# Performance work log

Measured on AMD Instinct MI355X. Metric: run time of the kernel, lower is better.

## Reference

```python
import jax, jax.numpy as jnp
import numpy as np

N_NODES = 100000
N_EDGES = 1600000
INPUT_DIM = 512
HIDDEN = 64
N_LAYERS = 3


def setup_inputs() -> dict:
    key = jax.random.key(0)
    ks = jax.random.split(key, 8)
    s = 0.05
    return {
        "x": jax.random.normal(ks[0], (N_NODES, INPUT_DIM), jnp.float32),
        "edge_index": jax.random.randint(ks[1], (2, N_EDGES), 0, N_NODES, jnp.int64),
        "W_enc": jax.random.normal(ks[2], (INPUT_DIM, HIDDEN), jnp.float32) * s,
        "b_enc": jnp.zeros((HIDDEN,), jnp.float32),
        "Wl": jax.random.normal(ks[3], (N_LAYERS, HIDDEN, HIDDEN), jnp.float32) * s,
        "bl": jnp.zeros((N_LAYERS, HIDDEN), jnp.float32),
        "Wr": jax.random.normal(ks[4], (N_LAYERS, HIDDEN, HIDDEN), jnp.float32) * s,
        "W_cls": jax.random.normal(ks[5], (HIDDEN, 1), jnp.float32) * s,
        "b_cls": jnp.zeros((1,), jnp.float32),
    }


def reference(x, edge_index, W_enc, b_enc, Wl, bl, Wr, W_cls, b_cls):
    # node encoder
    h = x @ W_enc + b_enc  # [N, H]
    N = h.shape[0]
    src, dst = edge_index[0], edge_index[1]  # messages flow src -> dst (PyG convention)
    ones = jnp.ones((src.shape[0],), h.dtype)
    deg = jax.ops.segment_sum(ones, dst, num_segments=N)  # in-degree per node
    inv_deg = jnp.where(deg > 0, 1.0 / jnp.maximum(deg, 1.0), 0.0)[:, None]
    n_layers = Wl.shape[0]
    for l in range(n_layers):
        # SAGEConv: mean-aggregate neighbor features, transform, add root transform
        msgs = h[src]  # [E, H] gather
        agg = jax.ops.segment_sum(msgs, dst, num_segments=N) * inv_deg  # mean aggr
        h_new = agg @ Wl[l] + bl[l] + h @ Wr[l]
        h = jax.nn.relu(h + h_new)  # residual + relu
    out = jax.nn.sigmoid(h @ W_cls + b_cls)  # [N, 1]
    return out.squeeze(-1)
```

## Files before the change

### kernel.cpp

```cpp
#include <hip/hip_runtime.h>
#include <math.h>

#define HID 64
#define KIN 512
#define NBK_MAX 256

typedef __attribute__((ext_vector_type(8))) short short8;
typedef __attribute__((ext_vector_type(4))) float floatx4;
typedef __attribute__((ext_vector_type(2))) float floatx2;

__device__ inline unsigned bf16pair(float a, float b) {
  unsigned ua = __float_as_uint(a);
  unsigned ub = __float_as_uint(b);
  ua = (ua + 0x7FFFu + ((ua >> 16) & 1u)) >> 16;
  ub = (ub + 0x7FFFu + ((ub >> 16) & 1u)) >> 16;
  return ua | (ub << 16);
}
__device__ inline unsigned short bf16one(float a) {
  unsigned ua = __float_as_uint(a);
  return (unsigned short)((ua + 0x7FFFu + ((ua >> 16) & 1u)) >> 16);
}
__device__ inline unsigned char fp8q(float a) {
  const int pk = __builtin_amdgcn_cvt_pk_fp8_f32(a, a, 0, false);
  return (unsigned char)(pk & 0xff);
}

__global__ __launch_bounds__(1024) void prep_bucket_kernel(
    const float* __restrict__ We, const float* __restrict__ Wl,
    const float* __restrict__ Wr, unsigned short* __restrict__ wte,
    unsigned short* __restrict__ wlrt, const int* __restrict__ src,
    const int* __restrict__ dst, int* __restrict__ gcur,
    unsigned* __restrict__ ebuf, int E, int N, int NBK, int CAP) {
  const int blk = blockIdx.x;
  const int tid = threadIdx.x;
  if (blk < 32) {
    const int t = blk * 1024 + tid;
    const int c = t >> 9, k = t & 511;
    wte[c * KIN + k] = bf16one(We[k * HID + c]);
    return;
  }
  if (blk < 56) {
    const int t = (blk - 32) * 1024 + tid;
    if (t < 24576) {
      const int mat = t >> 12;
      const int e = t & 4095;
      const int c = e >> 6, k = e & 63;
      const float* sp = (mat < 3) ? (Wl + (size_t)mat * 4096)
                                  : (Wr + (size_t)(mat - 3) * 4096);
      wlrt[(size_t)mat * 4096 + c * 64 + k] = bf16one(sp[k * 64 + c]);
    }
    return;
  }
  __shared__ int hist[NBK_MAX];
  __shared__ int bbase[NBK_MAX];
  __shared__ int curloc[NBK_MAX];
  const int e0 = (blk - 56) * 4096;
  for (int i = tid; i < NBK; i += 1024) {
    hist[i] = 0;
    curloc[i] = 0;
  }
  __syncthreads();
  int bk[4];
  unsigned pk[4];
#pragma unroll
  for (int u = 0; u < 4; u++) {
    const int e = e0 + u * 1024 + tid;
    bk[u] = -1;
    pk[u] = 0;
    if (e < E) {
      const int d = dst[e];
      if ((unsigned)d < (unsigned)N) {
        int s = src[e];
        if ((unsigned)s >= (unsigned)N) s = 0;
        bk[u] = d >> 9;
        pk[u] = ((unsigned)s << 9) | (unsigned)(d & 511);
        atomicAdd(&hist[bk[u]], 1);
      }
    }
  }
  __syncthreads();
  for (int i = tid; i < NBK; i += 1024)
    if (hist[i]) bbase[i] = atomicAdd(&gcur[i], hist[i]);
  __syncthreads();
#pragma unroll
  for (int u = 0; u < 4; u++) {
    if (bk[u] >= 0) {
      const int gp = bbase[bk[u]] + atomicAdd(&curloc[bk[u]], 1);
      if (gp < CAP) ebuf[(size_t)bk[u] * CAP + gp] = pk[u];
    }
  }
}

__global__ __launch_bounds__(256) void scatter_enc_kernel(
    const unsigned* __restrict__ ebuf, const int* __restrict__ gcur,
    int* __restrict__ row_start, float* __restrict__ inv_deg,
    int* __restrict__ csr_src, const float* __restrict__ x,
    const unsigned short* __restrict__ wt, const float* __restrict__ b,
    unsigned short* __restrict__ hb, unsigned char* __restrict__ h8, int N,
    int NBK, int CAP) {
  __shared__ __align__(16) unsigned char smem[16384];
  if (blockIdx.x < (unsigned)NBK) {
    int* cur = (int*)smem;
    int* rsl = (int*)(smem + 2048);
    int* psc = (int*)(smem + 4096);
    int* soffp = (int*)(smem + 5120);
    const int bkt = blockIdx.x;
    const int nodeBase = bkt << 9;
    const int tid = threadIdx.x;
    cur[tid] = 0;
    cur[tid + 256] = 0;
    __syncthreads();
    int cnt_b = gcur[bkt];
    if (cnt_b > CAP) cnt_b = CAP;
    const unsigned* eb = ebuf + (size_t)bkt * CAP;
    for (int i = tid; i < cnt_b; i += 256) atomicAdd(&cur[eb[i] & 511], 1);
    if (tid < 64) {
      int s = 0;
      for (int b2 = tid; b2 < bkt; b2 += 64) s += gcur[b2];
#pragma unroll
      for (int off = 32; off > 0; off >>= 1) s += __shfl_down(s, off, 64);
      if (tid == 0) *soffp = s;
    }
    __syncthreads();
    const int d0 = cur[2 * tid];
    const int d1 = cur[2 * tid + 1];
    psc[tid] = d0 + d1;
    __syncthreads();
    for (int off = 1; off < 256; off <<= 1) {
      int t = (tid >= off) ? psc[tid - off] : 0;
      __syncthreads();
      psc[tid] += t;
      __syncthreads();
    }
    const int soff = *soffp;
    const int base0 = soff + psc[tid] - (d0 + d1);
    rsl[2 * tid] = base0;
    rsl[2 * tid + 1] = base0 + d0;
    const int g0 = nodeBase + 2 * tid;
    const int g1 = g0 + 1;
    if (g0 < N) {
      row_start[g0] = base0;
      inv_deg[g0] = d0 ? 1.0f / (float)d0 : 0.f;
    }
    if (g1 < N) {
      row_start[g1] = base0 + d0;
      inv_deg[g1] = d1 ? 1.0f / (float)d1 : 0.f;
    }
    if (bkt == NBK - 1 && tid == 255) row_start[N] = soff + psc[255];
    cur[tid] = 0;
    cur[tid + 256] = 0;
    __syncthreads();
    for (int i = tid; i < cnt_b; i += 256) {
      const unsigned p = eb[i];
      const int dl = p & 511;
      const int pos = rsl[dl] + atomicAdd(&cur[dl], 1);
      csr_src[pos] = (int)(p >> 9);
    }
    return;
  }
  uint4(*sx)[256] = (uint4(*)[256])smem;
  uint4(*sw)[256] = (uint4(*)[256])(smem + 8192);
  const int t = threadIdx.x;
  const int lane = t & 63;
  const int wid = t >> 6;
  const int m15 = lane & 15;
  const int quad = lane >> 4;
  const int blockBase = (blockIdx.x - NBK) * 64;

  const int rs = t >> 2;
  const int qs = t & 3;
  const int us = rs * 4 + (qs ^ ((rs >> 1) & 3));
  const int gn = blockBase + rs;
  const bool valid = gn < N;
  const float* xp = x + (size_t)(valid ? gn : 0) * KIN + qs * 8;
  const unsigned short* wp = wt + (size_t)rs * KIN + qs * 8;

  const int arow = wid * 16 + m15;
  const int ua = arow * 4 + (quad ^ ((arow >> 1) & 3));
  int ub[4];
#pragma unroll
  for (int c4 = 0; c4 < 4; c4++) {
    const int col = c4 * 16 + m15;
    ub[c4] = col * 4 + (quad ^ ((col >> 1) & 3));
  }

  floatx4 acc[4];
#pragma unroll
  for (int c4 = 0; c4 < 4; c4++)
#pragma unroll
    for (int j = 0; j < 4; j++) acc[c4][j] = 0.f;

  float4 fx0, fx1;
  uint4 wv;
  if (valid) {
    fx0 = *(const float4*)(xp);
    fx1 = *(const float4*)(xp + 4);
  } else {
    fx0 = fx1 = make_float4(0.f, 0.f, 0.f, 0.f);
  }
  wv = *(const uint4*)(wp);

  for (int kc = 0; kc < 16; kc++) {
    const int curb = kc & 1;
    uint4 xu;
    xu.x = bf16pair(fx0.x, fx0.y);
    xu.y = bf16pair(fx0.z, fx0.w);
    xu.z = bf16pair(fx1.x, fx1.y);
    xu.w = bf16pair(fx1.z, fx1.w);
    sx[curb][us] = xu;
    sw[curb][us] = wv;
    __syncthreads();
    if (kc < 15) {
      const int ko = (kc + 1) * 32;
      if (valid) {
        fx0 = *(const float4*)(xp + ko);
        fx1 = *(const float4*)(xp + ko + 4);
      }
      wv = *(const uint4*)(wp + ko);
    }
    const short8 a = __builtin_bit_cast(short8, sx[curb][ua]);
#pragma unroll
    for (int c4 = 0; c4 < 4; c4++) {
      const short8 bf = __builtin_bit_cast(short8, sw[curb][ub[c4]]);
      acc[c4] =
          __builtin_amdgcn_mfma_f32_16x16x32_bf16(a, bf, acc[c4], 0, 0, 0);
    }
  }

#pragma unroll
  for (int c4 = 0; c4 < 4; c4++) {
    const float bias = b[c4 * 16 + m15];
#pragma unroll
    for (int r = 0; r < 4; r++) {
      const int row = blockBase + wid * 16 + quad * 4 + r;
      if (row < N) {
        const float v = acc[c4][r] + bias;
        hb[(size_t)row * HID + c4 * 16 + m15] = bf16one(v);
        h8[(size_t)row * HID + c4 * 16 + m15] = fp8q(v);
      }
    }
  }
}

__global__ __launch_bounds__(256) void layer_kernel(
    const unsigned short* __restrict__ hin,
    const unsigned char* __restrict__ h8in, unsigned short* __restrict__ hout,
    unsigned char* __restrict__ h8out, const int* __restrict__ row_start,
    const int* __restrict__ csr_src, const float* __restrict__ inv_deg,
    const unsigned short* __restrict__ Wlt,
    const unsigned short* __restrict__ Wrt, const float* __restrict__ bl,
    const float* __restrict__ Wc, const float* __restrict__ bc,
    float* __restrict__ out, int N) {
  __shared__ uint4 sAgg[512];
  __shared__ uint4 sH[512];
  __shared__ uint4 sWl[512];
  __shared__ uint4 sWr[512];
  const int tid = threadIdx.x;
  const int lane = tid & 63;
  const int wid = tid >> 6;
  const int m15 = lane & 15;
  const int quad = lane >> 4;
  const int blockBase = blockIdx.x * 64;

  {
    const int r = tid >> 2;
    const int gp = tid & 3;
    const int g0 = gp * 2, g1 = gp * 2 + 1;
    const int u0 = r * 8 + (g0 ^ (r & 7));
    const int u1 = r * 8 + (g1 ^ (r & 7));
    const int gn = blockBase + r;
    if (gn < N) {
      const uint4* hp = (const uint4*)(hin + (size_t)gn * HID);
      sH[u0] = hp[g0];
      sH[u1] = hp[g1];
    } else {
      const uint4 z = make_uint4(0, 0, 0, 0);
      sH[u0] = z;
      sH[u1] = z;
    }
    const uint4* wl = (const uint4*)(Wlt + (size_t)r * HID);
    const uint4* wr = (const uint4*)(Wrt + (size_t)r * HID);
    sWl[u0] = wl[g0];
    sWl[u1] = wl[g1];
    sWr[u0] = wr[g0];
    sWr[u1] = wr[g1];
  }

  {
    const int slot = lane >> 2;
    const int qc = lane & 3;
    const int nl = wid * 16 + slot;
    const int gn = blockBase + nl;
    float a[16];
#pragma unroll
    for (int c = 0; c < 16; c++) a[c] = 0.f;
    float id = 0.f;
    if (gn < N) {
      id = inv_deg[gn];
      const int s = row_start[gn];
      const int e = row_start[gn + 1];
      for (int j = s; j < e; j += 8) {
        int n[8];
        bool ok[8];
#pragma unroll
        for (int u = 0; u < 8; u++) {
          const int jj = j + u;
          ok[u] = jj < e;
          n[u] = csr_src[ok[u] ? jj : j];
        }
        uint4 v[8];
#pragma unroll
        for (int u = 0; u < 8; u++) {
          v[u] = *(const uint4*)(h8in + (size_t)n[u] * HID + qc * 16);
        }
#pragma unroll
        for (int u = 0; u < 8; u++) {
          if (!ok[u]) v[u] = make_uint4(0, 0, 0, 0);
#if __has_builtin(__builtin_amdgcn_cvt_pk_f32_fp8)
          {
            floatx2 p;
            p = __builtin_amdgcn_cvt_pk_f32_fp8((int)v[u].x, false);
            a[0] += p[0]; a[1] += p[1];
            p = __builtin_amdgcn_cvt_pk_f32_fp8((int)v[u].x, true);
            a[2] += p[0]; a[3] += p[1];
            p = __builtin_amdgcn_cvt_pk_f32_fp8((int)v[u].y, false);
            a[4] += p[0]; a[5] += p[1];
            p = __builtin_amdgcn_cvt_pk_f32_fp8((int)v[u].y, true);
            a[6] += p[0]; a[7] += p[1];
            p = __builtin_amdgcn_cvt_pk_f32_fp8((int)v[u].z, false);
            a[8] += p[0]; a[9] += p[1];
            p = __builtin_amdgcn_cvt_pk_f32_fp8((int)v[u].z, true);
            a[10] += p[0]; a[11] += p[1];
            p = __builtin_amdgcn_cvt_pk_f32_fp8((int)v[u].w, false);
            a[12] += p[0]; a[13] += p[1];
            p = __builtin_amdgcn_cvt_pk_f32_fp8((int)v[u].w, true);
            a[14] += p[0]; a[15] += p[1];
          }
#else
          a[0] += __builtin_amdgcn_cvt_f32_fp8(v[u].x, 0);
          a[1] += __builtin_amdgcn_cvt_f32_fp8(v[u].x, 1);
          a[2] += __builtin_amdgcn_cvt_f32_fp8(v[u].x, 2);
          a[3] += __builtin_amdgcn_cvt_f32_fp8(v[u].x, 3);
          a[4] += __builtin_amdgcn_cvt_f32_fp8(v[u].y, 0);
          a[5] += __builtin_amdgcn_cvt_f32_fp8(v[u].y, 1);
          a[6] += __builtin_amdgcn_cvt_f32_fp8(v[u].y, 2);
          a[7] += __builtin_amdgcn_cvt_f32_fp8(v[u].y, 3);
          a[8] += __builtin_amdgcn_cvt_f32_fp8(v[u].z, 0);
          a[9] += __builtin_amdgcn_cvt_f32_fp8(v[u].z, 1);
          a[10] += __builtin_amdgcn_cvt_f32_fp8(v[u].z, 2);
          a[11] += __builtin_amdgcn_cvt_f32_fp8(v[u].z, 3);
          a[12] += __builtin_amdgcn_cvt_f32_fp8(v[u].w, 0);
          a[13] += __builtin_amdgcn_cvt_f32_fp8(v[u].w, 1);
          a[14] += __builtin_amdgcn_cvt_f32_fp8(v[u].w, 2);
          a[15] += __builtin_amdgcn_cvt_f32_fp8(v[u].w, 3);
#endif
        }
      }
    }
    uint4 p0, p1;
    p0.x = bf16pair(a[0] * id, a[1] * id);
    p0.y = bf16pair(a[2] * id, a[3] * id);
    p0.z = bf16pair(a[4] * id, a[5] * id);
    p0.w = bf16pair(a[6] * id, a[7] * id);
    p1.x = bf16pair(a[8] * id, a[9] * id);
    p1.y = bf16pair(a[10] * id, a[11] * id);
    p1.z = bf16pair(a[12] * id, a[13] * id);
    p1.w = bf16pair(a[14] * id, a[15] * id);
    sAgg[nl * 8 + ((qc * 2) ^ (nl & 7))] = p0;
    sAgg[nl * 8 + ((qc * 2 + 1) ^ (nl & 7))] = p1;
  }
  __syncthreads();

  floatx4 acc[4];
#pragma unroll
  for (int c4 = 0; c4 < 4; c4++)
#pragma unroll
    for (int j = 0; j < 4; j++) acc[c4][j] = 0.f;

  const int arow = wid * 16 + m15;
#pragma unroll
  for (int c = 0; c < 2; c++) {
    const int ua = arow * 8 + ((c * 4 + quad) ^ (arow & 7));
    const short8 aA = __builtin_bit_cast(short8, sAgg[ua]);
    const short8 aH = __builtin_bit_cast(short8, sH[ua]);
#pragma unroll
    for (int c4 = 0; c4 < 4; c4++) {
      const int col = c4 * 16 + m15;
      const int ub = col * 8 + ((c * 4 + quad) ^ (col & 7));
      acc[c4] = __builtin_amdgcn_mfma_f32_16x16x32_bf16(
          aA, __builtin_bit_cast(short8, sWl[ub]), acc[c4], 0, 0, 0);
      acc[c4] = __builtin_amdgcn_mfma_f32_16x16x32_bf16(
          aH, __builtin_bit_cast(short8, sWr[ub]), acc[c4], 0, 0, 0);
    }
  }

  float vals[4][4];
#pragma unroll
  for (int c4 = 0; c4 < 4; c4++) {
    const float bias = bl[c4 * 16 + m15];
#pragma unroll
    for (int r = 0; r < 4; r++) {
      const int rowl = wid * 16 + quad * 4 + r;
      const unsigned short hv =
          ((const unsigned short*)
               sH)[(rowl * 8 + ((c4 * 2 + (m15 >> 3)) ^ (rowl & 7))) * 8 +
                   (m15 & 7)];
      const float v = __uint_as_float((unsigned)hv << 16) + acc[c4][r] + bias;
      vals[c4][r] = v > 0.f ? v : 0.f;
    }
  }
#pragma unroll
  for (int c4 = 0; c4 < 4; c4++) {
#pragma unroll
    for (int r = 0; r < 4; r++) {
      const int rowg = blockBase + wid * 16 + quad * 4 + r;
      if (rowg < N)
        hout[(size_t)rowg * HID + c4 * 16 + m15] = bf16one(vals[c4][r]);
    }
  }
  if (h8out != nullptr) {
#pragma unroll
    for (int c4 = 0; c4 < 4; c4++) {
#pragma unroll
      for (int r = 0; r < 4; r++) {
        const int rowg = blockBase + wid * 16 + quad * 4 + r;
        if (rowg < N)
          h8out[(size_t)rowg * HID + c4 * 16 + m15] = fp8q(vals[c4][r]);
      }
    }
  }
  if (Wc != nullptr) {
    float p[4] = {0.f, 0.f, 0.f, 0.f};
#pragma unroll
    for (int c4 = 0; c4 < 4; c4++) {
      const float wc = Wc[c4 * 16 + m15];
#pragma unroll
      for (int r = 0; r < 4; r++) p[r] += vals[c4][r] * wc;
    }
#pragma unroll
    for (int off = 1; off < 16; off <<= 1) {
#pragma unroll
      for (int r = 0; r < 4; r++) p[r] += __shfl_xor(p[r], off, 16);
    }
    if (m15 == 0) {
      const float bb = bc[0];
#pragma unroll
      for (int r = 0; r < 4; r++) {
        const int rowg = blockBase + wid * 16 + quad * 4 + r;
        if (rowg < N) out[rowg] = 1.0f / (1.0f + expf(-(p[r] + bb)));
      }
    }
  }
}

extern "C" void kernel_launch(void* const* d_in, const int* in_sizes, int n_in,
                              void* d_out, int out_size, void* d_ws,
                              size_t ws_size, hipStream_t stream) {
  const float* x = (const float*)d_in[0];
  const int* ei = (const int*)d_in[1];
  const float* W_enc = (const float*)d_in[2];
  const float* b_enc = (const float*)d_in[3];
  const float* Wl = (const float*)d_in[4];
  const float* bl = (const float*)d_in[5];
  const float* Wr = (const float*)d_in[6];
  const float* Wc = (const float*)d_in[7];
  const float* bc = (const float*)d_in[8];
  float* out = (float*)d_out;

  const int N = in_sizes[0] / KIN;
  const int E = in_sizes[1] / 2;
  const int* src = ei;
  const int* dst = ei + E;

  const int NBK = (N + 511) >> 9;
  int CAP = E / (NBK > 0 ? NBK : 1);
  CAP = CAP + (CAP >> 1) + 1024;
  CAP = (CAP + 255) & ~255;

  char* ws = (char*)d_ws;
  size_t off = 0;
  auto alloc = [&](size_t bytes) -> void* {
    void* p = ws + off;
    off += (bytes + 255) & ~(size_t)255;
    return p;
  };
  unsigned short* hb0 =
      (unsigned short*)alloc((size_t)N * HID * sizeof(unsigned short));
  unsigned short* hb1 =
      (unsigned short*)alloc((size_t)N * HID * sizeof(unsigned short));
  unsigned char* h8a = (unsigned char*)alloc((size_t)N * HID);
  unsigned char* h8b = (unsigned char*)alloc((size_t)N * HID);
  int* gcur = (int*)alloc((size_t)NBK * sizeof(int));
  int* row_start = (int*)alloc((size_t)(N + 1) * sizeof(int));
  float* inv_deg = (float*)alloc((size_t)N * sizeof(float));
  int* csr_src = (int*)alloc((size_t)E * sizeof(int));
  unsigned* ebuf = (unsigned*)alloc((size_t)NBK * CAP * sizeof(unsigned));
  unsigned short* wte =
      (unsigned short*)alloc((size_t)HID * KIN * sizeof(unsigned short));
  unsigned short* wlrt =
      (unsigned short*)alloc((size_t)6 * HID * HID * sizeof(unsigned short));

  hipMemsetAsync(gcur, 0, (size_t)NBK * sizeof(int), stream);

  const int nbktA = (E + 4095) / 4096;
  prep_bucket_kernel<<<56 + nbktA, 1024, 0, stream>>>(
      W_enc, Wl, Wr, wte, wlrt, src, dst, gcur, ebuf, E, N, NBK, CAP);
  const int nb64 = (N + 63) / 64;
  scatter_enc_kernel<<<NBK + nb64, 256, 0, stream>>>(
      ebuf, gcur, row_start, inv_deg, csr_src, x, wte, b_enc, hb0, h8a, N, NBK,
      CAP);

  layer_kernel<<<nb64, 256, 0, stream>>>(hb0, h8a, hb1, h8b, row_start, csr_src,
                                         inv_deg, wlrt, wlrt + 3 * 4096, bl,
                                         nullptr, nullptr, nullptr, N);
  layer_kernel<<<nb64, 256, 0, stream>>>(hb1, h8b, hb0, h8a, row_start, csr_src,
                                         inv_deg, wlrt + 4096, wlrt + 4 * 4096,
                                         bl + 64, nullptr, nullptr, nullptr, N);
  layer_kernel<<<nb64, 256, 0, stream>>>(hb0, h8a, hb1, nullptr, row_start,
                                         csr_src, inv_deg, wlrt + 2 * 4096,
                                         wlrt + 5 * 4096, bl + 128, Wc, bc, out,
                                         N);
}
```

Before: 431.5 us.

## Load encoder MFMA operands directly from global memory, dropping LDS staging

The encoder GEMM no longer stages x and W tiles through shared memory with double buffering and block barriers. Each lane loads its MFMA A and B fragments straight from global memory and converts x to bf16 in registers, with the K loop unrolled by four. Shared memory shrinks to the small CSR-build arrays, which may allow more resident blocks. In exchange, each wave reloads the full weight matrix on its own instead of sharing it across the block, and x loads are strided per lane rather than coalesced row loads.

```diff
diff --git a/kernel.cpp b/kernel.cpp
--- a/kernel.cpp
+++ b/kernel.cpp
@@ -98,12 +98,11 @@
     const unsigned short* __restrict__ wt, const float* __restrict__ b,
     unsigned short* __restrict__ hb, unsigned char* __restrict__ h8, int N,
     int NBK, int CAP) {
-  __shared__ __align__(16) unsigned char smem[16384];
+  __shared__ int cur[512];
+  __shared__ int rsl[512];
+  __shared__ int psc[256];
+  __shared__ int soffp;
   if (blockIdx.x < (unsigned)NBK) {
-    int* cur = (int*)smem;
-    int* rsl = (int*)(smem + 2048);
-    int* psc = (int*)(smem + 4096);
-    int* soffp = (int*)(smem + 5120);
     const int bkt = blockIdx.x;
     const int nodeBase = bkt << 9;
     const int tid = threadIdx.x;
@@ -119,7 +118,7 @@
       for (int b2 = tid; b2 < bkt; b2 += 64) s += gcur[b2];
 #pragma unroll
       for (int off = 32; off > 0; off >>= 1) s += __shfl_down(s, off, 64);
-      if (tid == 0) *soffp = s;
+      if (tid == 0) soffp = s;
     }
     __syncthreads();
     const int d0 = cur[2 * tid];
@@ -132,7 +131,7 @@
       psc[tid] += t;
       __syncthreads();
     }
-    const int soff = *soffp;
+    const int soff = soffp;
     const int base0 = soff + psc[tid] - (d0 + d1);
     rsl[2 * tid] = base0;
     rsl[2 * tid + 1] = base0 + d0;
@@ -158,8 +157,6 @@
     }
     return;
   }
-  uint4(*sx)[256] = (uint4(*)[256])smem;
-  uint4(*sw)[256] = (uint4(*)[256])(smem + 8192);
   const int t = threadIdx.x;
   const int lane = t & 63;
   const int wid = t >> 6;
@@ -167,22 +164,13 @@
   const int quad = lane >> 4;
   const int blockBase = (blockIdx.x - NBK) * 64;
 
-  const int rs = t >> 2;
-  const int qs = t & 3;
-  const int us = rs * 4 + (qs ^ ((rs >> 1) & 3));
-  const int gn = blockBase + rs;
-  const bool valid = gn < N;
-  const float* xp = x + (size_t)(valid ? gn : 0) * KIN + qs * 8;
-  const unsigned short* wp = wt + (size_t)rs * KIN + qs * 8;
-
-  const int arow = wid * 16 + m15;
-  const int ua = arow * 4 + (quad ^ ((arow >> 1) & 3));
-  int ub[4];
-#pragma unroll
-  for (int c4 = 0; c4 < 4; c4++) {
-    const int col = c4 * 16 + m15;
-    ub[c4] = col * 4 + (quad ^ ((col >> 1) & 3));
-  }
+  const int arow = blockBase + wid * 16 + m15;
+  const bool valid = arow < N;
+  const float* xp = x + (size_t)(valid ? arow : 0) * KIN + quad * 8;
+  const unsigned short* wp0 = wt + (size_t)m15 * KIN + quad * 8;
+  const unsigned short* wp1 = wp0 + (size_t)16 * KIN;
+  const unsigned short* wp2 = wp0 + (size_t)32 * KIN;
+  const unsigned short* wp3 = wp0 + (size_t)48 * KIN;
 
   floatx4 acc[4];
 #pragma unroll
@@ -190,41 +178,33 @@
 #pragma unroll
     for (int j = 0; j < 4; j++) acc[c4][j] = 0.f;
 
-  float4 fx0, fx1;
-  uint4 wv;
-  if (valid) {
-    fx0 = *(const float4*)(xp);
-    fx1 = *(const float4*)(xp + 4);
-  } else {
-    fx0 = fx1 = make_float4(0.f, 0.f, 0.f, 0.f);
-  }
-  wv = *(const uint4*)(wp);
-
+#pragma unroll 4
   for (int kc = 0; kc < 16; kc++) {
-    const int curb = kc & 1;
+    float4 fx0, fx1;
+    if (valid) {
+      fx0 = *(const float4*)(xp + kc * 32);
+      fx1 = *(const float4*)(xp + kc * 32 + 4);
+    } else {
+      fx0 = fx1 = make_float4(0.f, 0.f, 0.f, 0.f);
+    }
     uint4 xu;
     xu.x = bf16pair(fx0.x, fx0.y);
     xu.y = bf16pair(fx0.z, fx0.w);
     xu.z = bf16pair(fx1.x, fx1.y);
     xu.w = bf16pair(fx1.z, fx1.w);
-    sx[curb][us] = xu;
-    sw[curb][us] = wv;
-    __syncthreads();
-    if (kc < 15) {
-      const int ko = (kc + 1) * 32;
-      if (valid) {
-        fx0 = *(const float4*)(xp + ko);
-        fx1 = *(const float4*)(xp + ko + 4);
-      }
-      wv = *(const uint4*)(wp + ko);
-    }
-    const short8 a = __builtin_bit_cast(short8, sx[curb][ua]);
-#pragma unroll
-    for (int c4 = 0; c4 < 4; c4++) {
-      const short8 bf = __builtin_bit_cast(short8, sw[curb][ub[c4]]);
-      acc[c4] =
-          __builtin_amdgcn_mfma_f32_16x16x32_bf16(a, bf, acc[c4], 0, 0, 0);
-    }
+    const short8 a = __builtin_bit_cast(short8, xu);
+    const uint4 wv0 = *(const uint4*)(wp0 + kc * 32);
+    const uint4 wv1 = *(const uint4*)(wp1 + kc * 32);
+    const uint4 wv2 = *(const uint4*)(wp2 + kc * 32);
+    const uint4 wv3 = *(const uint4*)(wp3 + kc * 32);
+    acc[0] = __builtin_amdgcn_mfma_f32_16x16x32_bf16(
+        a, __builtin_bit_cast(short8, wv0), acc[0], 0, 0, 0);
+    acc[1] = __builtin_amdgcn_mfma_f32_16x16x32_bf16(
+        a, __builtin_bit_cast(short8, wv1), acc[1], 0, 0, 0);
+    acc[2] = __builtin_amdgcn_mfma_f32_16x16x32_bf16(
+        a, __builtin_bit_cast(short8, wv2), acc[2], 0, 0, 0);
+    acc[3] = __builtin_amdgcn_mfma_f32_16x16x32_bf16(
+        a, __builtin_bit_cast(short8, wv3), acc[3], 0, 0, 0);
   }
 
 #pragma unroll
```

Measured after the change: 471.3 us. 1.09x slower.
